# Performance work log

Hardware: AMD Instinct MI355X
Metric: run time of the kernel (lower is better)

Reference implementation:

```python
import jax, jax.numpy as jnp
import numpy as np

B, S, D, H = 4, 128, 512, 8
DH = D // H  # 64


def _heads(t):
    # [B,S,D] -> [B*H, S, DH]
    return t.reshape(B, S, H, DH).transpose(0, 2, 1, 3).reshape(B * H, S, DH)


def setup_inputs() -> dict:
    key = jax.random.key(0)
    ks = jax.random.split(key, 15)
    lim = np.sqrt(6.0 / (DH + DH))  # xavier_uniform fan for cubic tensor (torch uses first two dims)
    inp = {
        'x': jax.random.normal(ks[0], (B, S, D), jnp.float32),
        'y': jax.random.normal(ks[1], (B, S, D), jnp.float32),
        'z': jax.random.normal(ks[2], (B, S, D), jnp.float32),
        'B_weights': jax.random.uniform(ks[3], (DH, DH, DH), jnp.float32, -lim, lim),
    }
    s = 1.0 / np.sqrt(D)
    for i, nm in enumerate(['q', 'k1', 'k2', 'v1', 'v2']):
        inp['W' + nm] = jax.random.uniform(ks[4 + 2 * i], (D, D), jnp.float32, -s, s)
        inp['b' + nm] = jax.random.uniform(ks[5 + 2 * i], (D,), jnp.float32, -s, s)
    return inp


def reference(x, y, z, B_weights, Wq, bq, Wk1, bk1, Wk2, bk2, Wv1, bv1, Wv2, bv2):
    q = _heads(x @ Wq + bq)
    k1 = _heads(y @ Wk1 + bk1)
    v1 = _heads(y @ Wv1 + bv1)
    k2 = _heads(z @ Wk2 + bk2)
    v2 = _heads(z @ Wv2 + bv2)

    qk1 = jnp.einsum('aib,ajb->aij', q, k1)
    qk2 = jnp.einsum('aib,akb->aik', q, k2)
    k1k2 = jnp.einsum('ajb,akb->ajk', k1, k2)
    k2k2 = jnp.einsum('akc,akc->ak', k2, k2)
    qq = jnp.einsum('aib,aib->ai', q, q)
    k1k1 = jnp.einsum('ajb,ajb->aj', k1, k1)

    # cubic [A, S, S, S] tensor, A = B*H
    pre = (jnp.square(qk1)[:, :, :, None] * k2k2[:, None, None, :]
           + jnp.square(k1k2)[:, None, :, :] * qq[:, :, None, None]
           + jnp.square(qk2)[:, :, None, :] * k1k1[:, None, :, None]
           - 2.0 * qk1[:, :, :, None] * qk2[:, :, None, :] * k1k2[:, None, :, :])
    pre = jnp.where(jnp.isinf(pre), jnp.float32(55500.0), pre)
    logits = jnp.sqrt(pre)

    # joint softmax over last two axes (j,k)
    m = jnp.max(logits, axis=(-2, -1), keepdims=True)
    e = jnp.exp(logits - m)
    a = e / jnp.sum(e, axis=(-2, -1), keepdims=True)

    Bvj = jnp.einsum('qrs,ajr->aqsj', B_weights, v1)
    Bvjvk = jnp.einsum('aqsj,aks->aqjk', Bvj, v2)
    out = jnp.einsum('aijk,aqjk->aiq', a, Bvjvk)

    # [B*H, S, DH] -> [B, S, D]
    return out.reshape(B, H, S, DH).transpose(0, 2, 1, 3).reshape(B, S, D)
```

## Files before the change

kernel.cpp:

```cpp
#include <hip/hip_runtime.h>
#include <math.h>

#define Pq     0
#define Pk1    262144
#define Pk2    524288
#define Pv1    786432
#define Pv2    1048576
#define Oqk1   1310720
#define Oqk2   1835008
#define Ok1k2  2359296
#define Oqq    2883584
#define Ok1k1  2887680
#define Ok2k2  2891776
#define OU     2895872

#define LOG2E 1.44269504f

typedef _Float16 f16x8 __attribute__((ext_vector_type(8)));
typedef float    f32x4 __attribute__((ext_vector_type(4)));

__device__ __forceinline__ float block_reduce_max(float v, float* s_red) {
    #pragma unroll
    for (int o = 32; o > 0; o >>= 1) v = fmaxf(v, __shfl_down(v, o, 64));
    int wid = threadIdx.x >> 6;
    if ((threadIdx.x & 63) == 0) s_red[wid] = v;
    __syncthreads();
    if (threadIdx.x == 0)
        s_red[4] = fmaxf(fmaxf(s_red[0], s_red[1]), fmaxf(s_red[2], s_red[3]));
    __syncthreads();
    return s_red[4];
}

__device__ __forceinline__ float block_reduce_sum(float v, float* s_red) {
    #pragma unroll
    for (int o = 32; o > 0; o >>= 1) v += __shfl_down(v, o, 64);
    int wid = threadIdx.x >> 6;
    if ((threadIdx.x & 63) == 0) s_red[wid] = v;
    __syncthreads();
    if (threadIdx.x == 0)
        s_red[4] = s_red[0] + s_red[1] + s_red[2] + s_red[3];
    __syncthreads();
    return s_red[4];
}

__global__ __launch_bounds__(256) void k_proj(
    const float* __restrict__ x, const float* __restrict__ y, const float* __restrict__ z,
    const float* __restrict__ Wq,  const float* __restrict__ bq,
    const float* __restrict__ Wk1, const float* __restrict__ bk1,
    const float* __restrict__ Wk2, const float* __restrict__ bk2,
    const float* __restrict__ Wv1, const float* __restrict__ bv1,
    const float* __restrict__ Wv2, const float* __restrict__ bv2,
    float* __restrict__ ws)
{
    int p = blockIdx.z;
    const float *src, *W, *bias; float* dst;
    switch (p) {
        case 0:  src = x; W = Wq;  bias = bq;  dst = ws + Pq;  break;
        case 1:  src = y; W = Wk1; bias = bk1; dst = ws + Pk1; break;
        case 2:  src = z; W = Wk2; bias = bk2; dst = ws + Pk2; break;
        case 3:  src = y; W = Wv1; bias = bv1; dst = ws + Pv1; break;
        default: src = z; W = Wv2; bias = bv2; dst = ws + Pv2; break;
    }
    int m0 = blockIdx.y * 64;
    int n0 = blockIdx.x * 64;
    __shared__ float As[64 * 36];
    __shared__ float Bs[32 * 68];
    int t  = threadIdx.x;
    int tx = t & 15, ty = t >> 4;
    float acc[4][4] = {};
    for (int kt = 0; kt < 512; kt += 32) {
        #pragma unroll
        for (int r = 0; r < 2; ++r) {
            int f = t + 256 * r;
            int row = f >> 3, c4 = (f & 7) * 4;
            *(float4*)&As[row * 36 + c4] = *(const float4*)&src[(m0 + row) * 512 + kt + c4];
        }
        #pragma unroll
        for (int r = 0; r < 2; ++r) {
            int f = t + 256 * r;
            int row = f >> 4, c4 = (f & 15) * 4;
            *(float4*)&Bs[row * 68 + c4] = *(const float4*)&W[(kt + row) * 512 + n0 + c4];
        }
        __syncthreads();
        #pragma unroll
        for (int kk = 0; kk < 32; ++kk) {
            float a0 = As[(ty * 4 + 0) * 36 + kk];
            float a1 = As[(ty * 4 + 1) * 36 + kk];
            float a2 = As[(ty * 4 + 2) * 36 + kk];
            float a3 = As[(ty * 4 + 3) * 36 + kk];
            float4 b = *(const float4*)&Bs[kk * 68 + tx * 4];
            acc[0][0] += a0 * b.x; acc[0][1] += a0 * b.y; acc[0][2] += a0 * b.z; acc[0][3] += a0 * b.w;
            acc[1][0] += a1 * b.x; acc[1][1] += a1 * b.y; acc[1][2] += a1 * b.z; acc[1][3] += a1 * b.w;
            acc[2][0] += a2 * b.x; acc[2][1] += a2 * b.y; acc[2][2] += a2 * b.z; acc[2][3] += a2 * b.w;
            acc[3][0] += a3 * b.x; acc[3][1] += a3 * b.y; acc[3][2] += a3 * b.z; acc[3][3] += a3 * b.w;
        }
        __syncthreads();
    }
    float4 b4 = *(const float4*)&bias[n0 + tx * 4];
    int hd  = n0 >> 6;
    if (p >= 3) {
        int b_ = m0 >> 7;
        int aa = b_ * 8 + hd;
        int seq0 = (m0 & 127) + ty * 4;
        int cs = seq0 >> 3, os = seq0 & 7;
        char* dstb = (char*)dst + aa * 16384;
        const float bb[4] = { b4.x, b4.y, b4.z, b4.w };
        #pragma unroll
        for (int dd = 0; dd < 4; ++dd) {
            int dh = tx * 4 + dd;
            union { _Float16 f[4]; ushort4 u; } pk;
            pk.f[0] = (_Float16)(acc[0][dd] + bb[dd]);
            pk.f[1] = (_Float16)(acc[1][dd] + bb[dd]);
            pk.f[2] = (_Float16)(acc[2][dd] + bb[dd]);
            pk.f[3] = (_Float16)(acc[3][dd] + bb[dd]);
            *(ushort4*)(dstb + dh * 256 + ((cs ^ (dh & 7)) * 16) + os * 2) = pk.u;
        }
    } else {
        int dh0 = tx * 4;
        #pragma unroll
        for (int mm = 0; mm < 4; ++mm) {
            int row = m0 + ty * 4 + mm;
            int b_ = row >> 7, s = row & 127;
            float4 o;
            o.x = acc[mm][0] + b4.x; o.y = acc[mm][1] + b4.y;
            o.z = acc[mm][2] + b4.z; o.w = acc[mm][3] + b4.w;
            *(float4*)&dst[((b_ * 8 + hd) * 128 + s) * 64 + dh0] = o;
        }
    }
}

__global__ __launch_bounds__(256) void k_dots(float* ws)
{
    int a = blockIdx.x, mat = blockIdx.y;
    const float *lhs, *rhs; float* dst;
    if (mat == 0)      { lhs = ws + Pq  + a * 8192; rhs = ws + Pk1 + a * 8192; dst = ws + Oqk1  + a * 16384; }
    else if (mat == 1) { lhs = ws + Pq  + a * 8192; rhs = ws + Pk2 + a * 8192; dst = ws + Oqk2  + a * 16384; }
    else               { lhs = ws + Pk1 + a * 8192; rhs = ws + Pk2 + a * 8192; dst = ws + Ok1k2 + a * 16384; }
    float scl = (mat == 2) ? 1.f : LOG2E;
    __shared__ float Ls[128 * 65];
    __shared__ float Rs[128 * 65];
    int t = threadIdx.x;
    for (int r = 0; r < 8; ++r) {
        int f = t + 256 * r;
        int row = f >> 4, c4 = (f & 15) * 4;
        float4 v = *(const float4*)&lhs[row * 64 + c4];
        Ls[row * 65 + c4 + 0] = v.x; Ls[row * 65 + c4 + 1] = v.y;
        Ls[row * 65 + c4 + 2] = v.z; Ls[row * 65 + c4 + 3] = v.w;
        v = *(const float4*)&rhs[row * 64 + c4];
        Rs[row * 65 + c4 + 0] = v.x; Rs[row * 65 + c4 + 1] = v.y;
        Rs[row * 65 + c4 + 2] = v.z; Rs[row * 65 + c4 + 3] = v.w;
    }
    __syncthreads();
    int tx = t & 15, ty = t >> 4;
    float acc[8][8] = {};
    for (int dh = 0; dh < 64; ++dh) {
        float lv[8], rv[8];
        #pragma unroll
        for (int jj = 0; jj < 8; ++jj) lv[jj] = Ls[(ty * 8 + jj) * 65 + dh];
        #pragma unroll
        for (int kk = 0; kk < 8; ++kk) rv[kk] = Rs[(tx * 8 + kk) * 65 + dh];
        #pragma unroll
        for (int jj = 0; jj < 8; ++jj)
            #pragma unroll
            for (int kk = 0; kk < 8; ++kk)
                acc[jj][kk] += lv[jj] * rv[kk];
    }
    #pragma unroll
    for (int jj = 0; jj < 8; ++jj) {
        #pragma unroll
        for (int k4 = 0; k4 < 2; ++k4) {
            float4 o;
            o.x = acc[jj][k4 * 4 + 0] * scl; o.y = acc[jj][k4 * 4 + 1] * scl;
            o.z = acc[jj][k4 * 4 + 2] * scl; o.w = acc[jj][k4 * 4 + 3] * scl;
            *(float4*)&dst[(ty * 8 + jj) * 128 + tx * 8 + k4 * 4] = o;
        }
    }
    if (mat == 0) {
        if (t < 128) {
            float s = 0;
            for (int dh = 0; dh < 64; ++dh) { float v = Ls[t * 65 + dh]; s += v * v; }
            ws[Oqq + a * 128 + t] = s * (LOG2E * LOG2E);
        } else {
            int row = t - 128; float s = 0;
            for (int dh = 0; dh < 64; ++dh) { float v = Rs[row * 65 + dh]; s += v * v; }
            ws[Ok1k1 + a * 128 + row] = s;
        }
    } else if (mat == 1 && t >= 128) {
        int row = t - 128; float s = 0;
        for (int dh = 0; dh < 64; ++dh) { float v = Rs[row * 65 + dh]; s += v * v; }
        ws[Ok2k2 + a * 128 + row] = s;
    }
}

__global__ __launch_bounds__(256) void k_main(float* ws)
{
    int i = blockIdx.x, a = blockIdx.y;
    const float* gk1k2 = ws + Ok1k2 + a * 16384;
    __shared__ __align__(16) _Float16 s_v1t[8192];
    __shared__ __align__(16) _Float16 s_v2t[8192];
    __shared__ __align__(16) _Float16 s_Tt[8192];
    __shared__ __align__(16) float s_qk1[128];
    __shared__ __align__(16) float s_qk2[128];
    __shared__ __align__(16) float s_k1k1[128];
    __shared__ __align__(16) float s_k2k2[128];
    __shared__ float s_red[8];
    int t = threadIdx.x;
    int lane = t & 63, w = t >> 6;

    {
        const char* g1 = (const char*)(ws + Pv1) + a * 16384;
        const char* g2 = (const char*)(ws + Pv2) + a * 16384;
        #pragma unroll
        for (int c = 0; c < 4; ++c) {
            int ub = w * 4096 + c * 1024;
            int go = ub + lane * 16;
            __builtin_amdgcn_global_load_lds(
                (const __attribute__((address_space(1))) uint32_t*)(g1 + go),
                (__attribute__((address_space(3))) uint32_t*)((char*)s_v1t + ub), 16, 0, 0);
            __builtin_amdgcn_global_load_lds(
                (const __attribute__((address_space(1))) uint32_t*)(g2 + go),
                (__attribute__((address_space(3))) uint32_t*)((char*)s_v2t + ub), 16, 0, 0);
        }
    }
    if (t < 128) {
        s_qk1[t]  = ws[Oqk1 + a * 16384 + i * 128 + t];
        s_qk2[t]  = ws[Oqk2 + a * 16384 + i * 128 + t];
        s_k1k1[t] = ws[Ok1k1 + a * 128 + t];
        s_k2k2[t] = ws[Ok2k2 + a * 128 + t];
    }
    float qq = ws[Oqq + a * 128 + i];
    __syncthreads();

    int jb = w * 32;
    int lr = lane & 15;
    int lg = lane >> 4;
    int j0 = jb + lr, j1 = jb + 16 + lr;
    float c1_0 = s_qk1[j0], c1_1 = s_qk1[j1];
    float n1_0 = s_k1k1[j0], n1_1 = s_k1k1[j1];

    float lgt[4][16];
    float tmax = -INFINITY;
    #pragma unroll
    for (int kt = 0; kt < 4; ++kt) {
        int kb = kt * 32 + lg * 8;
        float c2v[8], n2v[8], g0v[8], g1v[8];
        *(float4*)&c2v[0] = *(const float4*)&s_qk2[kb];
        *(float4*)&c2v[4] = *(const float4*)&s_qk2[kb + 4];
        *(float4*)&n2v[0] = *(const float4*)&s_k2k2[kb];
        *(float4*)&n2v[4] = *(const float4*)&s_k2k2[kb + 4];
        *(float4*)&g0v[0] = *(const float4*)&gk1k2[j0 * 128 + kb];
        *(float4*)&g0v[4] = *(const float4*)&gk1k2[j0 * 128 + kb + 4];
        *(float4*)&g1v[0] = *(const float4*)&gk1k2[j1 * 128 + kb];
        *(float4*)&g1v[4] = *(const float4*)&gk1k2[j1 * 128 + kb + 4];
        #pragma unroll
        for (int u = 0; u < 8; ++u) {
            float c2 = c2v[u], n2 = n2v[u], c2sq = c2 * c2;
            float g = g0v[u];
            float pre = c1_0 * c1_0 * n2 + g * g * qq + c2sq * n1_0 - 2.f * c1_0 * c2 * g;
            float l0 = sqrtf(fmaxf(pre, 0.f));
            g = g1v[u];
            pre = c1_1 * c1_1 * n2 + g * g * qq + c2sq * n1_1 - 2.f * c1_1 * c2 * g;
            float l1 = sqrtf(fmaxf(pre, 0.f));
            lgt[kt][u] = l0; lgt[kt][8 + u] = l1;
            tmax = fmaxf(tmax, fmaxf(l0, l1));
        }
    }
    float m2 = block_reduce_max(tmax, s_red);

    f32x4 accT[2][4] = {};
    float Zp = 0.f;
    #pragma unroll
    for (int kt = 0; kt < 4; ++kt) {
        union { _Float16 f[8]; f16x8 v; } ea0, ea1;
        #pragma unroll
        for (int u = 0; u < 8; ++u) {
            float e0 = exp2f(lgt[kt][u]     - m2);
            float e1 = exp2f(lgt[kt][8 + u] - m2);
            Zp += e0 + e1;
            ea0.f[u] = (_Float16)e0;
            ea1.f[u] = (_Float16)e1;
        }
        int cb = kt * 4 + lg;
        #pragma unroll
        for (int nt = 0; nt < 4; ++nt) {
            int dh = nt * 16 + lr;
            f16x8 bV = *(const f16x8*)((const char*)s_v2t + dh * 256 + ((cb ^ (dh & 7)) * 16));
            accT[0][nt] = __builtin_amdgcn_mfma_f32_16x16x32_f16(ea0.v, bV, accT[0][nt], 0, 0, 0);
            accT[1][nt] = __builtin_amdgcn_mfma_f32_16x16x32_f16(ea1.v, bV, accT[1][nt], 0, 0, 0);
        }
    }

    #pragma unroll
    for (int mt = 0; mt < 2; ++mt) {
        int jw = jb + mt * 16 + lg * 4;
        int cj = jw >> 3, oj = jw & 7;
        #pragma unroll
        for (int nt = 0; nt < 4; ++nt) {
            int s = nt * 16 + lr;
            union { _Float16 f[4]; ushort4 u; } pk;
            f32x4 v = accT[mt][nt];
            pk.f[0] = (_Float16)v[0]; pk.f[1] = (_Float16)v[1];
            pk.f[2] = (_Float16)v[2]; pk.f[3] = (_Float16)v[3];
            *(ushort4*)((char*)s_Tt + s * 256 + ((cj ^ (s & 7)) * 16) + oj * 2) = pk.u;
        }
    }
    float Z = block_reduce_sum(Zp, s_red);

    f32x4 accU[4] = {};
    int r = w * 16 + lr;
    #pragma unroll
    for (int ks = 0; ks < 4; ++ks) {
        int cj = ks * 4 + lg;
        f16x8 aV = *(const f16x8*)((const char*)s_v1t + r * 256 + ((cj ^ (r & 7)) * 16));
        #pragma unroll
        for (int nt = 0; nt < 4; ++nt) {
            int s = nt * 16 + lr;
            f16x8 bT = *(const f16x8*)((const char*)s_Tt + s * 256 + ((cj ^ (s & 7)) * 16));
            accU[nt] = __builtin_amdgcn_mfma_f32_16x16x32_f16(aV, bT, accU[nt], 0, 0, 0);
        }
    }
    float invZ = 1.f / Z;
    ushort* gU = (ushort*)(ws + OU) + (size_t)(a * 128 + i) * 4096;
    #pragma unroll
    for (int nt = 0; nt < 4; ++nt) {
        int s = nt * 16 + lr;
        #pragma unroll
        for (int reg = 0; reg < 4; ++reg) {
            int rr = w * 16 + lg * 4 + reg;
            union { _Float16 h; ushort u; } cv;
            cv.h = (_Float16)(accU[nt][reg] * invZ);
            gU[rr * 64 + s] = cv.u;
        }
    }
}

__global__ __launch_bounds__(256) void k_bgemm(const float* __restrict__ Bw, float* ws)
{
    int m0 = blockIdx.x * 64;
    int ks = blockIdx.y * 512;
    const ushort* U16 = (const ushort*)(ws + OU);
    float* gP = ws + blockIdx.y * 262144;
    __shared__ __align__(16) ushort sB[64 * 512];
    int t = threadIdx.x;
    int lane = t & 63, w = t >> 6;

    {
        int q = t >> 2, kc = (t & 3) * 128;
        const float* src = Bw + q * 4096 + ks + kc;
        char* base = (char*)sB + q * 1024;
        #pragma unroll
        for (int g2 = 0; g2 < 16; ++g2) {
            float4 a4 = *(const float4*)&src[g2 * 8];
            float4 b4 = *(const float4*)&src[g2 * 8 + 4];
            union { _Float16 f[8]; f16x8 v; } pk;
            pk.f[0] = (_Float16)a4.x; pk.f[1] = (_Float16)a4.y;
            pk.f[2] = (_Float16)a4.z; pk.f[3] = (_Float16)a4.w;
            pk.f[4] = (_Float16)b4.x; pk.f[5] = (_Float16)b4.y;
            pk.f[6] = (_Float16)b4.z; pk.f[7] = (_Float16)b4.w;
            int c = (kc >> 3) + g2;
            *(f16x8*)(base + ((c ^ (q & 7)) * 16)) = pk.v;
        }
    }
    __syncthreads();

    int lr = lane & 15, lg = lane >> 4;
    int mrow = m0 + w * 16 + lr;
    const ushort* urow = U16 + (size_t)mrow * 4096 + ks + lg * 8;
    f32x4 acc[4] = {};
    #pragma unroll
    for (int kt = 0; kt < 16; ++kt) {
        f16x8 aU = *(const f16x8*)(urow + kt * 32);
        int c = kt * 4 + lg;
        #pragma unroll
        for (int nt = 0; nt < 4; ++nt) {
            int q = nt * 16 + lr;
            f16x8 bB = *(const f16x8*)((const char*)sB + q * 1024 + ((c ^ (q & 7)) * 16));
            acc[nt] = __builtin_amdgcn_mfma_f32_16x16x32_f16(aU, bB, acc[nt], 0, 0, 0);
        }
    }
    #pragma unroll
    for (int nt = 0; nt < 4; ++nt) {
        #pragma unroll
        for (int reg = 0; reg < 4; ++reg) {
            int m = m0 + w * 16 + lg * 4 + reg;
            gP[m * 64 + nt * 16 + lr] = acc[nt][reg];
        }
    }
}

__global__ __launch_bounds__(256) void k_reduce(const float* __restrict__ ws, float* __restrict__ out)
{
    int e0 = (blockIdx.x * 256 + threadIdx.x) * 4;
    float4 s = *(const float4*)&ws[e0];
    #pragma unroll
    for (int sp = 1; sp < 8; ++sp) {
        float4 v = *(const float4*)&ws[sp * 262144 + e0];
        s.x += v.x; s.y += v.y; s.z += v.z; s.w += v.w;
    }
    int m = e0 >> 6, q0 = e0 & 63;
    int a = m >> 7, i = m & 127;
    int b_ = a >> 3, h = a & 7;
    *(float4*)&out[b_ * 65536 + i * 512 + h * 64 + q0] = s;
}

extern "C" void kernel_launch(void* const* d_in, const int* in_sizes, int n_in,
                              void* d_out, int out_size, void* d_ws, size_t ws_size,
                              hipStream_t stream)
{
    const float* x   = (const float*)d_in[0];
    const float* y   = (const float*)d_in[1];
    const float* z   = (const float*)d_in[2];
    const float* Bw  = (const float*)d_in[3];
    const float* Wq  = (const float*)d_in[4];
    const float* bq  = (const float*)d_in[5];
    const float* Wk1 = (const float*)d_in[6];
    const float* bk1 = (const float*)d_in[7];
    const float* Wk2 = (const float*)d_in[8];
    const float* bk2 = (const float*)d_in[9];
    const float* Wv1 = (const float*)d_in[10];
    const float* bv1 = (const float*)d_in[11];
    const float* Wv2 = (const float*)d_in[12];
    const float* bv2 = (const float*)d_in[13];
    float* ws = (float*)d_ws;
    float* out = (float*)d_out;

    k_proj<<<dim3(8, 8, 5), 256, 0, stream>>>(x, y, z, Wq, bq, Wk1, bk1, Wk2, bk2,
                                              Wv1, bv1, Wv2, bv2, ws);
    k_dots<<<dim3(32, 3), 256, 0, stream>>>(ws);
    k_main<<<dim3(128, 32), 256, 0, stream>>>(ws);
    k_bgemm<<<dim3(64, 8), 256, 0, stream>>>(Bw, ws);
    k_reduce<<<256, 256, 0, stream>>>(ws, out);
}
```

Measured before the change: 216.5 us.

## Factor logit quadratic, use raw sqrt/exp intrinsics, alias V2 and T in LDS

Rewrites the cubic logit expression as a completed square in k1k2, so each element needs fewer FMAs, with per-row constants hoisted. Replaces sqrtf/exp2f/half conversions with raw v_sqrt_f32, v_exp_f32 and packed cvt_pkrtz instructions. Reuses one LDS buffer for both v2 and the intermediate T, moving the sum reduction before the T write and adding a barrier. This cuts LDS use and may raise occupancy. In exchange it adds division by qq, round-toward-zero fp16 conversion, and denormal/precision differences.

```diff
diff --git a/kernel.cpp b/kernel.cpp
--- a/kernel.cpp
+++ b/kernel.cpp
@@ -197,8 +197,7 @@
     int i = blockIdx.x, a = blockIdx.y;
     const float* gk1k2 = ws + Ok1k2 + a * 16384;
     __shared__ __align__(16) _Float16 s_v1t[8192];
-    __shared__ __align__(16) _Float16 s_v2t[8192];
-    __shared__ __align__(16) _Float16 s_Tt[8192];
+    __shared__ __align__(16) _Float16 s_kv[8192];
     __shared__ __align__(16) float s_qk1[128];
     __shared__ __align__(16) float s_qk2[128];
     __shared__ __align__(16) float s_k1k1[128];
@@ -219,7 +218,7 @@
                 (__attribute__((address_space(3))) uint32_t*)((char*)s_v1t + ub), 16, 0, 0);
             __builtin_amdgcn_global_load_lds(
                 (const __attribute__((address_space(1))) uint32_t*)(g2 + go),
-                (__attribute__((address_space(3))) uint32_t*)((char*)s_v2t + ub), 16, 0, 0);
+                (__attribute__((address_space(3))) uint32_t*)((char*)s_kv + ub), 16, 0, 0);
         }
     }
     if (t < 128) {
@@ -237,9 +236,14 @@
     int j0 = jb + lr, j1 = jb + 16 + lr;
     float c1_0 = s_qk1[j0], c1_1 = s_qk1[j1];
     float n1_0 = s_k1k1[j0], n1_1 = s_k1k1[j1];
+    float rq  = 1.0f / qq;
+    float na0 = -(c1_0 * rq), na1 = -(c1_1 * rq);
+    float be0 = fmaf(c1_0, na0, n1_0);
+    float be1 = fmaf(c1_1, na1, n1_1);
+    float sq0 = c1_0 * c1_0, sq1 = c1_1 * c1_1;
 
     float lgt[4][16];
-    float tmax = -INFINITY;
+    float tmax = 0.f;
     #pragma unroll
     for (int kt = 0; kt < 4; ++kt) {
         int kb = kt * 32 + lg * 8;
@@ -254,13 +258,17 @@
         *(float4*)&g1v[4] = *(const float4*)&gk1k2[j1 * 128 + kb + 4];
         #pragma unroll
         for (int u = 0; u < 8; ++u) {
-            float c2 = c2v[u], n2 = n2v[u], c2sq = c2 * c2;
-            float g = g0v[u];
-            float pre = c1_0 * c1_0 * n2 + g * g * qq + c2sq * n1_0 - 2.f * c1_0 * c2 * g;
-            float l0 = sqrtf(fmaxf(pre, 0.f));
-            g = g1v[u];
-            pre = c1_1 * c1_1 * n2 + g * g * qq + c2sq * n1_1 - 2.f * c1_1 * c2 * g;
-            float l1 = sqrtf(fmaxf(pre, 0.f));
+            float c2 = c2v[u], n2 = n2v[u];
+            float c2sq = c2 * c2;
+            float h0 = fmaf(be0, c2sq, sq0 * n2);
+            float h1 = fmaf(be1, c2sq, sq1 * n2);
+            float t0 = fmaf(na0, c2, g0v[u]);
+            float t1 = fmaf(na1, c2, g1v[u]);
+            float p0 = fmaxf(fmaf(qq * t0, t0, h0), 0.f);
+            float p1 = fmaxf(fmaf(qq * t1, t1, h1), 0.f);
+            float l0, l1;
+            asm("v_sqrt_f32 %0, %1" : "=v"(l0) : "v"(p0));
+            asm("v_sqrt_f32 %0, %1" : "=v"(l1) : "v"(p1));
             lgt[kt][u] = l0; lgt[kt][8 + u] = l1;
             tmax = fmaxf(tmax, fmaxf(l0, l1));
         }
@@ -271,24 +279,34 @@
     float Zp = 0.f;
     #pragma unroll
     for (int kt = 0; kt < 4; ++kt) {
-        union { _Float16 f[8]; f16x8 v; } ea0, ea1;
-        #pragma unroll
-        for (int u = 0; u < 8; ++u) {
-            float e0 = exp2f(lgt[kt][u]     - m2);
-            float e1 = exp2f(lgt[kt][8 + u] - m2);
-            Zp += e0 + e1;
-            ea0.f[u] = (_Float16)e0;
-            ea1.f[u] = (_Float16)e1;
+        union { f16x8 v; unsigned int u32[4]; } ea0, ea1;
+        #pragma unroll
+        for (int u = 0; u < 8; u += 2) {
+            float x0 = lgt[kt][u]     - m2, x1 = lgt[kt][u + 1]     - m2;
+            float x2 = lgt[kt][8 + u] - m2, x3 = lgt[kt][8 + u + 1] - m2;
+            float e0, e1, e2, e3;
+            asm("v_exp_f32 %0, %1" : "=v"(e0) : "v"(x0));
+            asm("v_exp_f32 %0, %1" : "=v"(e1) : "v"(x1));
+            asm("v_exp_f32 %0, %1" : "=v"(e2) : "v"(x2));
+            asm("v_exp_f32 %0, %1" : "=v"(e3) : "v"(x3));
+            Zp += (e0 + e1) + (e2 + e3);
+            unsigned int r01, r23;
+            asm("v_cvt_pkrtz_f16_f32 %0, %1, %2" : "=v"(r01) : "v"(e0), "v"(e1));
+            asm("v_cvt_pkrtz_f16_f32 %0, %1, %2" : "=v"(r23) : "v"(e2), "v"(e3));
+            ea0.u32[u >> 1] = r01;
+            ea1.u32[u >> 1] = r23;
         }
         int cb = kt * 4 + lg;
         #pragma unroll
         for (int nt = 0; nt < 4; ++nt) {
             int dh = nt * 16 + lr;
-            f16x8 bV = *(const f16x8*)((const char*)s_v2t + dh * 256 + ((cb ^ (dh & 7)) * 16));
+            f16x8 bV = *(const f16x8*)((const char*)s_kv + dh * 256 + ((cb ^ (dh & 7)) * 16));
             accT[0][nt] = __builtin_amdgcn_mfma_f32_16x16x32_f16(ea0.v, bV, accT[0][nt], 0, 0, 0);
             accT[1][nt] = __builtin_amdgcn_mfma_f32_16x16x32_f16(ea1.v, bV, accT[1][nt], 0, 0, 0);
         }
     }
+
+    float Z = block_reduce_sum(Zp, s_red);
 
     #pragma unroll
     for (int mt = 0; mt < 2; ++mt) {
@@ -301,10 +319,10 @@
             f32x4 v = accT[mt][nt];
             pk.f[0] = (_Float16)v[0]; pk.f[1] = (_Float16)v[1];
             pk.f[2] = (_Float16)v[2]; pk.f[3] = (_Float16)v[3];
-            *(ushort4*)((char*)s_Tt + s * 256 + ((cj ^ (s & 7)) * 16) + oj * 2) = pk.u;
-        }
-    }
-    float Z = block_reduce_sum(Zp, s_red);
+            *(ushort4*)((char*)s_kv + s * 256 + ((cj ^ (s & 7)) * 16) + oj * 2) = pk.u;
+        }
+    }
+    __syncthreads();
 
     f32x4 accU[4] = {};
     int r = w * 16 + lr;
@@ -315,7 +333,7 @@
         #pragma unroll
         for (int nt = 0; nt < 4; ++nt) {
             int s = nt * 16 + lr;
-            f16x8 bT = *(const f16x8*)((const char*)s_Tt + s * 256 + ((cj ^ (s & 7)) * 16));
+            f16x8 bT = *(const f16x8*)((const char*)s_kv + s * 256 + ((cj ^ (s & 7)) * 16));
             accU[nt] = __builtin_amdgcn_mfma_f32_16x16x32_f16(aV, bT, accU[nt], 0, 0, 0);
         }
     }
```

Measured after the change: 200.9 us. 1.08x faster.
